# Performance work log

Measured on AMD Instinct MI355X. Metric: run time of the kernel, lower is better.

The kernel has to match this reference:

```python
import jax, jax.numpy as jnp
from jax import lax
import numpy as np

NPOINT = 1024
RADIUS = 0.1
NSAMPLE = 32
BN_EPS = 1e-5


def _fps(xyz, npoint):
    # xyz: [B, N, 3]. Deterministic start at index 0 (torch uses randint seed).
    B, N, _ = xyz.shape

    def step(carry, _):
        dist, far = carry
        centroid = jnp.take_along_axis(xyz, far[:, None, None], axis=1)  # [B,1,3]
        d = jnp.sum((xyz - centroid) ** 2, axis=-1)                      # [B,N]
        dist = jnp.minimum(dist, d)
        nxt = jnp.argmax(dist, axis=-1).astype(jnp.int32)
        return (dist, nxt), far

    init = (jnp.full((B, N), 1e10, xyz.dtype), jnp.zeros((B,), jnp.int32))
    _, idx = lax.scan(step, init, None, length=npoint)
    return jnp.transpose(idx)  # [B, npoint]


def _sqdist(a, b):
    # a: [B,S,3], b: [B,N,3] -> [B,S,N]
    return (jnp.sum(a * a, -1)[:, :, None] + jnp.sum(b * b, -1)[:, None, :]
            - 2.0 * jnp.einsum('bsc,bnc->bsn', a, b))


def _gather(pts, idx):
    # pts: [B,N,C], idx: [B,...] int -> [B,...,C]
    B = pts.shape[0]
    flat = idx.reshape(B, -1)
    out = jnp.take_along_axis(pts, flat[..., None], axis=1)
    return out.reshape(idx.shape + (pts.shape[-1],))


def _ball_query(radius, nsample, xyz, new_xyz):
    B, N, _ = xyz.shape
    sq = _sqdist(new_xyz, xyz)                                        # [B,S,N]
    ar = jnp.arange(N, dtype=jnp.int32)[None, None, :]
    gi = jnp.where(sq > radius ** 2, N, ar)                           # out-of-ball -> N
    gi = jnp.sort(gi, axis=-1)[:, :, :nsample]                        # [B,S,K]
    first = gi[:, :, :1]
    return jnp.where(gi == N, first, gi)                              # pad with first


def _sa_forward(xyz, points, params):
    # torch layout in: xyz [B,3,N], points [B,D,N]
    xyz = jnp.transpose(xyz, (0, 2, 1))        # [B,N,3]
    points = jnp.transpose(points, (0, 2, 1))  # [B,N,D]
    fps_idx = lax.stop_gradient(_fps(xyz, NPOINT))          # [B,S]
    new_xyz = _gather(xyz, fps_idx)                          # [B,S,3]
    idx = _ball_query(RADIUS, NSAMPLE, xyz, new_xyz)         # [B,S,K]
    g_xyz = _gather(xyz, idx) - new_xyz[:, :, None, :]       # [B,S,K,3]
    g_pts = _gather(points, idx)                             # [B,S,K,D]
    x = jnp.concatenate([g_xyz, g_pts], axis=-1)             # [B,S,K,3+D]
    for (W, b, g, bt, m, v) in params:
        x = jnp.einsum('bskc,oc->bsko', x, W) + b            # 1x1 conv
        x = (x - m) * (g / jnp.sqrt(v + BN_EPS)) + bt        # eval-mode BN
        x = jax.nn.relu(x)
    feat = jnp.max(x, axis=2)                                # max over K -> [B,S,C']
    return jnp.transpose(feat, (0, 2, 1))                    # [B,C',S]


def setup_inputs() -> dict:
    key = jax.random.key(0)
    ks = jax.random.split(key, 16)
    B, N = 4, 8192
    d = {}
    d['xyz'] = jax.random.uniform(ks[0], (B, 3, N), jnp.float32)       # unit cube cloud
    d['points'] = jax.random.normal(ks[1], (B, 3, N), jnp.float32)     # e.g. normals
    dims = [(6, 64), (64, 64), (64, 128)]
    k = 2
    for li, (cin, cout) in enumerate(dims, start=1):
        d[f'w{li}'] = jax.random.normal(ks[k], (cout, cin), jnp.float32) * (1.0 / np.sqrt(cin)); k += 1
        d[f'b{li}'] = jnp.zeros((cout,), jnp.float32)
        d[f'g{li}'] = jnp.ones((cout,), jnp.float32)
        d[f't{li}'] = jnp.zeros((cout,), jnp.float32)
        d[f'm{li}'] = jax.random.normal(ks[k], (cout,), jnp.float32) * 0.01; k += 1
        d[f'v{li}'] = jnp.ones((cout,), jnp.float32)
    return d


def reference(xyz, points,
              w1, b1, g1, t1, m1, v1,
              w2, b2, g2, t2, m2, v2,
              w3, b3, g3, t3, m3, v3):
    params = [(w1, b1, g1, t1, m1, v1),
              (w2, b2, g2, t2, m2, v2),
              (w3, b3, g3, t3, m3, v3)]
    return _sa_forward(xyz, points, params)
```

## Files before the change

kernel.cpp:

```cpp
#include <hip/hip_runtime.h>
#include <math.h>

#define NPTS 8192
#define NPOINT 1024
#define NSAMPLE 32

typedef float v2f __attribute__((ext_vector_type(2)));

template <int CTRL>
__device__ __forceinline__ unsigned long long dpp_max_step(unsigned long long key) {
  int lo = (int)(unsigned)key;
  int hi = (int)(unsigned)(key >> 32);
  int slo = __builtin_amdgcn_update_dpp(0, lo, CTRL, 0xF, 0xF, true);
  int shi = __builtin_amdgcn_update_dpp(0, hi, CTRL, 0xF, 0xF, true);
  unsigned long long o =
      ((unsigned long long)(unsigned)shi << 32) | (unsigned)slo;
  return (o > key) ? o : key;
}

__global__ __launch_bounds__(256, 1) void fps_kernel(const float* __restrict__ xyz,
                                                     float* __restrict__ new_xyz) {
#pragma clang fp contract(off)
  const int b = blockIdx.x;
  const int tid = threadIdx.x;
  const float* xp = xyz + (size_t)b * 3 * NPTS;
  v2f px2[16], py2[16], pz2[16], d2[16];
#pragma unroll
  for (int j = 0; j < 16; ++j) {
    int n0 = tid + 512 * j;
    int n1 = n0 + 256;
    px2[j] = (v2f){xp[n0], xp[n1]};
    py2[j] = (v2f){xp[NPTS + n0], xp[NPTS + n1]};
    pz2[j] = (v2f){xp[2 * NPTS + n0], xp[2 * NPTS + n1]};
    d2[j] = (v2f){1e10f, 1e10f};
  }
  __shared__ unsigned long long red[2][4];
  float* outp = new_xyz + (size_t)b * NPOINT * 3;
  float cx = xp[0], cy = xp[NPTS], cz = xp[2 * NPTS];
  if (tid == 0) { outp[0] = cx; outp[1] = cy; outp[2] = cz; }
  for (int s = 1; s < NPOINT; ++s) {
    const v2f cxx = (v2f){cx, cx};
    const v2f cyy = (v2f){cy, cy};
    const v2f czz = (v2f){cz, cz};
    float bv = -1.0f;
    int bI = 0;
#pragma unroll
    for (int j = 0; j < 16; ++j) {
      v2f dx = px2[j] - cxx;
      v2f dy = py2[j] - cyy;
      v2f dz = pz2[j] - czz;
      v2f xx = dx * dx;
      v2f yy = dy * dy;
      v2f zz = dz * dz;
      v2f d = (xx + yy) + zz;
      float dmx = fminf(d2[j].x, d.x);
      float dmy = fminf(d2[j].y, d.y);
      d2[j].x = dmx;
      d2[j].y = dmy;
      if (dmx > bv) { bv = dmx; bI = 2 * j; }
      if (dmy > bv) { bv = dmy; bI = 2 * j + 1; }
    }
    int bi = tid + (bI << 8);
    unsigned long long key =
        ((unsigned long long)__float_as_uint(bv) << 32) |
        (unsigned)(8191 - bi);
    key = dpp_max_step<0x111>(key);
    key = dpp_max_step<0x112>(key);
    key = dpp_max_step<0x114>(key);
    key = dpp_max_step<0x118>(key);
    key = dpp_max_step<0x142>(key);
    key = dpp_max_step<0x143>(key);
    unsigned wlo = (unsigned)__builtin_amdgcn_readlane((int)(unsigned)key, 63);
    unsigned whi =
        (unsigned)__builtin_amdgcn_readlane((int)(unsigned)(key >> 32), 63);
    unsigned long long wkey = ((unsigned long long)whi << 32) | wlo;
    if ((tid & 63) == 0) red[s & 1][tid >> 6] = wkey;
    __syncthreads();
    unsigned long long k0 = red[s & 1][0];
    unsigned long long k1 = red[s & 1][1];
    unsigned long long k2 = red[s & 1][2];
    unsigned long long k3 = red[s & 1][3];
    unsigned long long ka = (k0 > k1) ? k0 : k1;
    unsigned long long kb = (k2 > k3) ? k2 : k3;
    unsigned long long km = (ka > kb) ? ka : kb;
    int gi = 8191 - (int)(unsigned)(km & 0xFFFFFFFFull);
    cx = xp[gi];
    cy = xp[NPTS + gi];
    cz = xp[2 * NPTS + gi];
    if (tid == 0) { outp[3 * s] = cx; outp[3 * s + 1] = cy; outp[3 * s + 2] = cz; }
  }
}

__global__ __launch_bounds__(256) void bq_kernel(const float* __restrict__ xyz,
                                                 const float* __restrict__ new_xyz,
                                                 int* __restrict__ idx_out) {
#pragma clang fp contract(off)
  __shared__ int slots[4][NSAMPLE];
  const int tid = threadIdx.x;
  const int wv = tid >> 6, lane = tid & 63;
  const int gc = blockIdx.x * 4 + wv;
  const int b = gc >> 10;
  const float* xp = xyz + (size_t)b * 3 * NPTS;
  const float* cp = new_xyz + (size_t)gc * 3;
  const float cx = cp[0], cy = cp[1], cz = cp[2];
  const float asq = (cx * cx + cy * cy) + cz * cz;
  int cnt = 0;
  for (int base = 0; base < NPTS; base += 64) {
    int n = base + lane;
    float x = xp[n], y = xp[NPTS + n], z = xp[2 * NPTS + n];
    float bsq = (x * x + y * y) + z * z;
    float ab = (x * cx + y * cy) + z * cz;
    float sq = (asq + bsq) - 2.0f * ab;
    bool inc = !(sq > 0.01f);
    unsigned long long mk = __ballot(inc);
    int pos = cnt + (int)__popcll(mk & ((1ull << lane) - 1ull));
    if (inc && pos < NSAMPLE) slots[wv][pos] = n;
    cnt += (int)__popcll(mk);
    if (cnt >= NSAMPLE) break;
  }
  __syncthreads();
  if (lane < NSAMPLE) {
    int first = slots[wv][0];
    int v = (lane < cnt) ? slots[wv][lane] : first;
    idx_out[(size_t)gc * NSAMPLE + lane] = v;
  }
}

__global__ __launch_bounds__(256) void setup_kernel(
    const float* __restrict__ w3,
    const float* __restrict__ b1, const float* __restrict__ g1, const float* __restrict__ t1,
    const float* __restrict__ m1, const float* __restrict__ v1,
    const float* __restrict__ b2, const float* __restrict__ g2, const float* __restrict__ t2,
    const float* __restrict__ m2, const float* __restrict__ v2,
    const float* __restrict__ b3, const float* __restrict__ g3, const float* __restrict__ t3,
    const float* __restrict__ m3, const float* __restrict__ v3,
    float* __restrict__ w3t, float* __restrict__ scsh) {
  int tid = threadIdx.x;
  for (int i = tid; i < 8192; i += 256) {
    int o = i >> 6, c = i & 63;
    w3t[c * 128 + o] = w3[i];
  }
  if (tid < 64) {
    float s = g1[tid] / sqrtf(v1[tid] + 1e-5f);
    scsh[tid] = s;
    scsh[64 + tid] = (b1[tid] - m1[tid]) * s + t1[tid];
    float s2 = g2[tid] / sqrtf(v2[tid] + 1e-5f);
    scsh[128 + tid] = s2;
    scsh[192 + tid] = (b2[tid] - m2[tid]) * s2 + t2[tid];
  }
  if (tid < 128) {
    float s3 = g3[tid] / sqrtf(v3[tid] + 1e-5f);
    scsh[256 + tid] = s3;
    scsh[384 + tid] = (b3[tid] - m3[tid]) * s3 + t3[tid];
  }
}

__global__ __launch_bounds__(256, 2) void mlp_kernel(
    const float* __restrict__ xyz, const float* __restrict__ points,
    const float* __restrict__ new_xyz, const int* __restrict__ idx,
    const float* __restrict__ w1, const float* __restrict__ w2,
    const float* __restrict__ w3t, const float* __restrict__ scsh,
    float* __restrict__ out) {
  __shared__ float act[256 * 64];
  float4* act4 = (float4*)act;
  const int tid = threadIdx.x;
  const int s0 = blockIdx.x * 8;
  const int b = s0 >> 10;
  const int g = tid >> 5;
  const int k = tid & 31;
  const int gc = s0 + g;
  const float* xp = xyz + (size_t)b * 3 * NPTS;
  const float* pp = points + (size_t)b * 3 * NPTS;
  const float* cp = new_xyz + (size_t)gc * 3;
  const int n = idx[(size_t)gc * NSAMPLE + k];
  float f0 = xp[n] - cp[0];
  float f1 = xp[NPTS + n] - cp[1];
  float f2 = xp[2 * NPTS + n] - cp[2];
  float f3 = pp[n];
  float f4 = pp[NPTS + n];
  float f5 = pp[2 * NPTS + n];
  const float* sc1 = scsh;        const float* sh1 = scsh + 64;
  const float* sc2 = scsh + 128;  const float* sh2 = scsh + 192;
  const float* sc3 = scsh + 256;  const float* sh3 = scsh + 384;
  const int row = tid;

#pragma unroll
  for (int oc = 0; oc < 16; ++oc) {
    float va[4];
#pragma unroll
    for (int jj = 0; jj < 4; ++jj) {
      int o = oc * 4 + jj;
      const float* wr = w1 + o * 6;
      float a = f0 * wr[0] + f1 * wr[1] + f2 * wr[2] +
                f3 * wr[3] + f4 * wr[4] + f5 * wr[5];
      va[jj] = fmaxf(a * sc1[o] + sh1[o], 0.f);
    }
    act4[row * 16 + (oc ^ (row & 15))] = make_float4(va[0], va[1], va[2], va[3]);
  }

  float acc[64];
#pragma unroll
  for (int o = 0; o < 64; ++o) acc[o] = 0.f;
  for (int cc = 0; cc < 16; ++cc) {
    float4 av = act4[row * 16 + (cc ^ (row & 15))];
#pragma unroll
    for (int o = 0; o < 64; ++o) {
      const float* wr = w2 + o * 64 + cc * 4;
      acc[o] += av.x * wr[0] + av.y * wr[1] + av.z * wr[2] + av.w * wr[3];
    }
  }
#pragma unroll
  for (int oc = 0; oc < 16; ++oc) {
    float va[4];
#pragma unroll
    for (int jj = 0; jj < 4; ++jj) {
      int o = oc * 4 + jj;
      va[jj] = fmaxf(acc[o] * sc2[o] + sh2[o], 0.f);
    }
    act4[row * 16 + (oc ^ (row & 15))] = make_float4(va[0], va[1], va[2], va[3]);
  }
  __syncthreads();

  const int j = k;
  const int sb = gc & 1023;
  for (int p = 0; p < 4; ++p) {
    int o3 = p * 32 + j;
    float wreg[64];
#pragma unroll
    for (int c = 0; c < 64; ++c) wreg[c] = w3t[c * 128 + o3];
    float osc = sc3[o3], osh = sh3[o3];
    float vmax = 0.f;
    for (int kk = 0; kk < 32; ++kk) {
      int r2 = g * 32 + kk;
      float a0 = 0.f, a1 = 0.f, a2 = 0.f, a3 = 0.f;
#pragma unroll
      for (int cc = 0; cc < 16; cc += 4) {
        float4 u0 = act4[r2 * 16 + ((cc + 0) ^ (r2 & 15))];
        float4 u1 = act4[r2 * 16 + ((cc + 1) ^ (r2 & 15))];
        float4 u2 = act4[r2 * 16 + ((cc + 2) ^ (r2 & 15))];
        float4 u3 = act4[r2 * 16 + ((cc + 3) ^ (r2 & 15))];
        a0 += u0.x * wreg[4*cc+0]  + u0.y * wreg[4*cc+1]  + u0.z * wreg[4*cc+2]  + u0.w * wreg[4*cc+3];
        a1 += u1.x * wreg[4*cc+4]  + u1.y * wreg[4*cc+5]  + u1.z * wreg[4*cc+6]  + u1.w * wreg[4*cc+7];
        a2 += u2.x * wreg[4*cc+8]  + u2.y * wreg[4*cc+9]  + u2.z * wreg[4*cc+10] + u2.w * wreg[4*cc+11];
        a3 += u3.x * wreg[4*cc+12] + u3.y * wreg[4*cc+13] + u3.z * wreg[4*cc+14] + u3.w * wreg[4*cc+15];
      }
      float x3 = (a0 + a1) + (a2 + a3);
      vmax = fmaxf(vmax, fmaxf(x3 * osc + osh, 0.f));
    }
    out[((size_t)b * 128 + o3) * 1024 + sb] = vmax;
  }
}

extern "C" void kernel_launch(void* const* d_in, const int* in_sizes, int n_in,
                              void* d_out, int out_size, void* d_ws, size_t ws_size,
                              hipStream_t stream) {
  (void)in_sizes; (void)n_in; (void)out_size; (void)ws_size;
  const float* xyz    = (const float*)d_in[0];
  const float* points = (const float*)d_in[1];
  const float* w1 = (const float*)d_in[2];
  const float* b1 = (const float*)d_in[3];
  const float* g1 = (const float*)d_in[4];
  const float* t1 = (const float*)d_in[5];
  const float* m1 = (const float*)d_in[6];
  const float* v1 = (const float*)d_in[7];
  const float* w2 = (const float*)d_in[8];
  const float* b2 = (const float*)d_in[9];
  const float* g2 = (const float*)d_in[10];
  const float* t2 = (const float*)d_in[11];
  const float* m2 = (const float*)d_in[12];
  const float* v2 = (const float*)d_in[13];
  const float* w3 = (const float*)d_in[14];
  const float* b3 = (const float*)d_in[15];
  const float* g3 = (const float*)d_in[16];
  const float* t3 = (const float*)d_in[17];
  const float* m3 = (const float*)d_in[18];
  const float* v3 = (const float*)d_in[19];

  float* wsf = (float*)d_ws;
  float* new_xyz = wsf;
  int*   idx     = (int*)(wsf + 12288);
  float* w3t     = wsf + 12288 + 131072;
  float* scsh    = w3t + 8192;
  float* out     = (float*)d_out;

  hipLaunchKernelGGL(setup_kernel, dim3(1), dim3(256), 0, stream,
                     w3, b1, g1, t1, m1, v1, b2, g2, t2, m2, v2,
                     b3, g3, t3, m3, v3, w3t, scsh);
  hipLaunchKernelGGL(fps_kernel, dim3(4), dim3(256), 0, stream, xyz, new_xyz);
  hipLaunchKernelGGL(bq_kernel, dim3(1024), dim3(256), 0, stream,
                     xyz, new_xyz, idx);
  hipLaunchKernelGGL(mlp_kernel, dim3(512), dim3(256), 0, stream,
                     xyz, points, new_xyz, idx, w1, w2, w3t, scsh, out);
}
```

Measured before the change: 1.294 ms.

## Split FPS wave argmax into float max then index max, pack xyz as float4

The wave-level argmax in the FPS loop now runs as a 32-bit float max reduction followed by a 32-bit index max over lanes holding the winning value. This replaces the earlier reduction over a 64-bit packed key, which needed two DPP moves and a 64-bit compare per step. The setup kernel now also repacks xyz into an interleaved float4 buffer, so each centroid fetch is one uniform vector load (index made wave-uniform with readfirstlane) instead of three strided loads. This adds a transpose pass over the input and a second DPP reduction chain in every FPS iteration.

```diff
diff --git a/kernel.cpp b/kernel.cpp
--- a/kernel.cpp
+++ b/kernel.cpp
@@ -8,35 +8,38 @@
 typedef float v2f __attribute__((ext_vector_type(2)));
 
 template <int CTRL>
-__device__ __forceinline__ unsigned long long dpp_max_step(unsigned long long key) {
-  int lo = (int)(unsigned)key;
-  int hi = (int)(unsigned)(key >> 32);
-  int slo = __builtin_amdgcn_update_dpp(0, lo, CTRL, 0xF, 0xF, true);
-  int shi = __builtin_amdgcn_update_dpp(0, hi, CTRL, 0xF, 0xF, true);
-  unsigned long long o =
-      ((unsigned long long)(unsigned)shi << 32) | (unsigned)slo;
-  return (o > key) ? o : key;
-}
-
-__global__ __launch_bounds__(256, 1) void fps_kernel(const float* __restrict__ xyz,
+__device__ __forceinline__ float dpp_fmax_step(float v) {
+  int s = __builtin_amdgcn_update_dpp(0, __float_as_int(v), CTRL, 0xF, 0xF, true);
+  return fmaxf(v, __int_as_float(s));
+}
+template <int CTRL>
+__device__ __forceinline__ unsigned dpp_umax_step(unsigned v) {
+  int s = __builtin_amdgcn_update_dpp(0, (int)v, CTRL, 0xF, 0xF, true);
+  unsigned u = (unsigned)s;
+  return (u > v) ? u : v;
+}
+
+__global__ __launch_bounds__(256, 1) void fps_kernel(const float4* __restrict__ xyz4,
                                                      float* __restrict__ new_xyz) {
 #pragma clang fp contract(off)
   const int b = blockIdx.x;
   const int tid = threadIdx.x;
-  const float* xp = xyz + (size_t)b * 3 * NPTS;
+  const float4* xp4 = xyz4 + (size_t)b * NPTS;
   v2f px2[16], py2[16], pz2[16], d2[16];
 #pragma unroll
   for (int j = 0; j < 16; ++j) {
     int n0 = tid + 512 * j;
-    int n1 = n0 + 256;
-    px2[j] = (v2f){xp[n0], xp[n1]};
-    py2[j] = (v2f){xp[NPTS + n0], xp[NPTS + n1]};
-    pz2[j] = (v2f){xp[2 * NPTS + n0], xp[2 * NPTS + n1]};
+    float4 a = xp4[n0];
+    float4 c2 = xp4[n0 + 256];
+    px2[j] = (v2f){a.x, c2.x};
+    py2[j] = (v2f){a.y, c2.y};
+    pz2[j] = (v2f){a.z, c2.z};
     d2[j] = (v2f){1e10f, 1e10f};
   }
   __shared__ unsigned long long red[2][4];
   float* outp = new_xyz + (size_t)b * NPOINT * 3;
-  float cx = xp[0], cy = xp[NPTS], cz = xp[2 * NPTS];
+  float4 c0 = xp4[0];
+  float cx = c0.x, cy = c0.y, cz = c0.z;
   if (tid == 0) { outp[0] = cx; outp[1] = cy; outp[2] = cz; }
   for (int s = 1; s < NPOINT; ++s) {
     const v2f cxx = (v2f){cx, cx};
@@ -61,32 +64,37 @@
       if (dmy > bv) { bv = dmy; bI = 2 * j + 1; }
     }
     int bi = tid + (bI << 8);
-    unsigned long long key =
-        ((unsigned long long)__float_as_uint(bv) << 32) |
-        (unsigned)(8191 - bi);
-    key = dpp_max_step<0x111>(key);
-    key = dpp_max_step<0x112>(key);
-    key = dpp_max_step<0x114>(key);
-    key = dpp_max_step<0x118>(key);
-    key = dpp_max_step<0x142>(key);
-    key = dpp_max_step<0x143>(key);
-    unsigned wlo = (unsigned)__builtin_amdgcn_readlane((int)(unsigned)key, 63);
-    unsigned whi =
-        (unsigned)__builtin_amdgcn_readlane((int)(unsigned)(key >> 32), 63);
-    unsigned long long wkey = ((unsigned long long)whi << 32) | wlo;
+    float m = bv;
+    m = dpp_fmax_step<0x111>(m);
+    m = dpp_fmax_step<0x112>(m);
+    m = dpp_fmax_step<0x114>(m);
+    m = dpp_fmax_step<0x118>(m);
+    m = dpp_fmax_step<0x142>(m);
+    m = dpp_fmax_step<0x143>(m);
+    float Mw = __int_as_float(__builtin_amdgcn_readlane(__float_as_int(m), 63));
+    unsigned k2 = (bv == Mw) ? (unsigned)(8191 - bi) : 0u;
+    k2 = dpp_umax_step<0x111>(k2);
+    k2 = dpp_umax_step<0x112>(k2);
+    k2 = dpp_umax_step<0x114>(k2);
+    k2 = dpp_umax_step<0x118>(k2);
+    k2 = dpp_umax_step<0x142>(k2);
+    k2 = dpp_umax_step<0x143>(k2);
+    unsigned K2 = (unsigned)__builtin_amdgcn_readlane((int)k2, 63);
+    unsigned long long wkey =
+        ((unsigned long long)__float_as_uint(Mw) << 32) | K2;
     if ((tid & 63) == 0) red[s & 1][tid >> 6] = wkey;
     __syncthreads();
     unsigned long long k0 = red[s & 1][0];
     unsigned long long k1 = red[s & 1][1];
-    unsigned long long k2 = red[s & 1][2];
+    unsigned long long kB = red[s & 1][2];
     unsigned long long k3 = red[s & 1][3];
     unsigned long long ka = (k0 > k1) ? k0 : k1;
-    unsigned long long kb = (k2 > k3) ? k2 : k3;
+    unsigned long long kb = (kB > k3) ? kB : k3;
     unsigned long long km = (ka > kb) ? ka : kb;
     int gi = 8191 - (int)(unsigned)(km & 0xFFFFFFFFull);
-    cx = xp[gi];
-    cy = xp[NPTS + gi];
-    cz = xp[2 * NPTS + gi];
+    int giu = __builtin_amdgcn_readfirstlane(gi);
+    float4 cc = xp4[giu];
+    cx = cc.x; cy = cc.y; cz = cc.z;
     if (tid == 0) { outp[3 * s] = cx; outp[3 * s + 1] = cy; outp[3 * s + 2] = cz; }
   }
 }
@@ -127,15 +135,20 @@
 }
 
 __global__ __launch_bounds__(256) void setup_kernel(
-    const float* __restrict__ w3,
+    const float* __restrict__ xyz, const float* __restrict__ w3,
     const float* __restrict__ b1, const float* __restrict__ g1, const float* __restrict__ t1,
     const float* __restrict__ m1, const float* __restrict__ v1,
     const float* __restrict__ b2, const float* __restrict__ g2, const float* __restrict__ t2,
     const float* __restrict__ m2, const float* __restrict__ v2,
     const float* __restrict__ b3, const float* __restrict__ g3, const float* __restrict__ t3,
     const float* __restrict__ m3, const float* __restrict__ v3,
-    float* __restrict__ w3t, float* __restrict__ scsh) {
+    float4* __restrict__ xyz4, float* __restrict__ w3t, float* __restrict__ scsh) {
   int tid = threadIdx.x;
+  int p = blockIdx.x * 256 + tid;
+  int bb = p >> 13, n = p & 8191;
+  const float* src = xyz + (size_t)bb * 3 * NPTS;
+  xyz4[p] = make_float4(src[n], src[NPTS + n], src[2 * NPTS + n], 0.f);
+  if (blockIdx.x != 0) return;
   for (int i = tid; i < 8192; i += 256) {
     int o = i >> 6, c = i & 63;
     w3t[c * 128 + o] = w3[i];
@@ -281,12 +294,13 @@
   int*   idx     = (int*)(wsf + 12288);
   float* w3t     = wsf + 12288 + 131072;
   float* scsh    = w3t + 8192;
+  float4* xyz4   = (float4*)(scsh + 512);
   float* out     = (float*)d_out;
 
-  hipLaunchKernelGGL(setup_kernel, dim3(1), dim3(256), 0, stream,
-                     w3, b1, g1, t1, m1, v1, b2, g2, t2, m2, v2,
-                     b3, g3, t3, m3, v3, w3t, scsh);
-  hipLaunchKernelGGL(fps_kernel, dim3(4), dim3(256), 0, stream, xyz, new_xyz);
+  hipLaunchKernelGGL(setup_kernel, dim3(128), dim3(256), 0, stream,
+                     xyz, w3, b1, g1, t1, m1, v1, b2, g2, t2, m2, v2,
+                     b3, g3, t3, m3, v3, xyz4, w3t, scsh);
+  hipLaunchKernelGGL(fps_kernel, dim3(4), dim3(256), 0, stream, xyz4, new_xyz);
   hipLaunchKernelGGL(bq_kernel, dim3(1024), dim3(256), 0, stream,
                      xyz, new_xyz, idx);
   hipLaunchKernelGGL(mlp_kernel, dim3(512), dim3(256), 0, stream,
```

Result: faster. 1.247 ms (-3.6%).
